# Optimization experiments

Hardware: AMD Instinct MI355X
Metric: run time of the kernel (lower is better)

Reference implementation:

```python
import jax, jax.numpy as jnp
import numpy as np

N_NODES = 81920
N_EDGES = 1310720
NODES_PER_GRAPH = 320
N_GRAPHS = N_NODES // NODES_PER_GRAPH  # 256
IN_DIM = 64
HID = 64
OUT = 64


def setup_inputs() -> dict:
    key = jax.random.key(0)
    ks = jax.random.split(key, 16)
    x = jax.random.normal(ks[0], (N_NODES, IN_DIM), dtype=jnp.float32)
    edge_index = jax.random.randint(ks[1], (2, N_EDGES), 0, N_NODES, dtype=jnp.int32)
    # sorted graph-membership vector: 256 graphs of 320 nodes each
    batch = (jnp.arange(N_NODES, dtype=jnp.int32) // NODES_PER_GRAPH)
    std = 1.0  # module re-inits nn.Linear weights with N(0, 1)
    dims = [(IN_DIM, HID), (HID, HID), (HID, OUT)]
    params = {}
    for i, (di, do) in enumerate(dims):
        params[f"Wl{i}"] = std * jax.random.normal(ks[2 + 3 * i], (di, do), dtype=jnp.float32)
        params[f"bl{i}"] = jnp.zeros((do,), dtype=jnp.float32)
        params[f"Wr{i}"] = std * jax.random.normal(ks[3 + 3 * i], (di, do), dtype=jnp.float32)
    return dict(x=x, edge_index=edge_index, batch=batch, **params)


def _sage_conv(x, src, dst, Wl, bl, Wr):
    # PyG SAGEConv (aggr='mean', root_weight=True):
    #   out = lin_l(mean_{j in N(i)} x_j) + lin_r(x_i)
    msg = x[src]                                              # [E, d] gather
    agg = jax.ops.segment_sum(msg, dst, num_segments=N_NODES)  # [N, d] scatter-add
    cnt = jax.ops.segment_sum(jnp.ones((src.shape[0],), x.dtype), dst,
                              num_segments=N_NODES)
    agg = agg / jnp.maximum(cnt, 1.0)[:, None]                # mean aggregation
    return agg @ Wl + bl + x @ Wr


def reference(x, edge_index, batch, Wl0, bl0, Wr0, Wl1, bl1, Wr1, Wl2, bl2, Wr2):
    src, dst = edge_index[0], edge_index[1]
    layers = [(Wl0, bl0, Wr0), (Wl1, bl1, Wr1), (Wl2, bl2, Wr2)]
    h = x
    for i, (Wl, bl, Wr) in enumerate(layers):
        h = _sage_conv(h, src, dst, Wl, bl, Wr)
        if i < len(layers) - 1:
            h = jax.nn.relu(h)
            # F.dropout is identity in eval mode (training=False)
    # unbatch + take node 0 of every graph: first index where batch == g
    first_idx = jnp.searchsorted(batch, jnp.arange(N_GRAPHS, dtype=batch.dtype))
    return h[first_idx]  # [N_GRAPHS, OUT]
```

## Files before the change

### kernel.cpp

```cpp
#include <hip/hip_runtime.h>

#define N_NODES 81920
#define N_EDGES 1310720
#define NG 256
#define D 64
#define TM 64
#define SA 65
#define SB 33
#define NB 320
#define NBLK 1280
#define BMW 2560
#define HCHUNK 4096
#define EPT 16
#define CAP0 1280
#define CAP1 256
#define CAP2 64

typedef __attribute__((ext_vector_type(2))) short sbf2;

__device__ __forceinline__ bool tb(const unsigned* bm, int i) {
    return (bm[i >> 5] >> (i & 31)) & 1u;
}
__device__ __forceinline__ unsigned bf16rne(float f) {
    unsigned u = __float_as_uint(f);
    return (u + 0x7fffu + ((u >> 16) & 1u)) >> 16;
}


__global__ __launch_bounds__(256) void init_ws(float4* __restrict__ aggb4,
                                               unsigned* __restrict__ bms,
                                               int* __restrict__ indeg,
                                               int* __restrict__ n01,
                                               int* __restrict__ cur0,
                                               int* __restrict__ cur1,
                                               int* __restrict__ cur2) {
    int t = blockIdx.x * 256 + threadIdx.x;
    float4 z = make_float4(0.f, 0.f, 0.f, 0.f);
    aggb4[t] = z;
    aggb4[t + NBLK * 256] = z;
    if (t < 3 * BMW) bms[t] = 0u;
    if (t < N_NODES) indeg[t] = 0;
    if (t < 2) n01[t] = 0;
    if (t < NBLK) {
        cur0[t] = t * CAP0;
        cur1[t] = t * CAP1;
        cur2[t] = t * CAP2;
    }
}


__global__ void ff_mark(const int* __restrict__ batch, int* __restrict__ fidx,
                        unsigned* __restrict__ bm2, unsigned* __restrict__ bm1,
                        float* __restrict__ aggf) {
    int i = blockIdx.x * 256 + threadIdx.x;
    int b = batch[i];
    if (i == 0 || batch[i - 1] != b) {
        fidx[b] = i;
        unsigned bit = 1u << (i & 31);
        atomicOr(&bm2[i >> 5], bit);
        atomicOr(&bm1[i >> 5], bit);
        float4* r = (float4*)&aggf[i * D];
        #pragma unroll
        for (int j = 0; j < 16; ++j) r[j] = make_float4(0.f, 0.f, 0.f, 0.f);
    }
}

__global__ void mark_srcs_bm(const int* __restrict__ src, const int* __restrict__ dst,
                             const unsigned* __restrict__ bmD, unsigned* __restrict__ bmS,
                             const unsigned* __restrict__ orsrc) {
    if (orsrc && blockIdx.x == 0) {
        for (int w = threadIdx.x; w < BMW; w += 256)
            if (orsrc[w]) atomicOr(&bmS[w], orsrc[w]);
    }
    int e = blockIdx.x * 256 + threadIdx.x;
    if (e < N_EDGES && tb(bmD, dst[e])) {
        int s = src[e];
        atomicOr(&bmS[s >> 5], 1u << (s & 31));
    }
}


__global__ __launch_bounds__(256) void build(const int* __restrict__ src,
                                             const int* __restrict__ dst,
                                             const unsigned* __restrict__ bm0,
                                             const unsigned* __restrict__ bm1,
                                             const unsigned* __restrict__ bm2,
                                             int* __restrict__ cur0,
                                             int* __restrict__ cur1,
                                             int* __restrict__ cur2,
                                             int* __restrict__ esp0,
                                             int* __restrict__ esp1,
                                             int* __restrict__ esp2,
                                             int* __restrict__ indeg,
                                             int* __restrict__ list1,
                                             int* __restrict__ n1) {
    __shared__ int h0[NBLK];
    __shared__ int b0[NBLK];
    const int tid = threadIdx.x;
    const int e0  = blockIdx.x * HCHUNK;

    for (int i = tid; i < NBLK; i += 256) h0[i] = 0;

    {
        int i = blockIdx.x * 256 + tid;
        int lane = tid & 63;
        bool p1 = tb(bm1, i);
        unsigned long long b1 = __ballot(p1);
        int lt = __popcll(b1 & ((1ull << lane) - 1));
        int base = 0;
        if (lane == 0 && b1) base = atomicAdd(n1, __popcll(b1));
        base = __shfl(base, 0);
        if (p1) list1[base + lt] = i;
    }
    __syncthreads();

    int pk_r[EPT];
    int sb_r[EPT];
    int rk_r[EPT];

    #pragma unroll
    for (int j = 0; j < EPT; ++j) {
        int e = e0 + j * 256 + tid;
        int d = dst[e];
        sb_r[j] = -1;
        if (tb(bm0, d)) {
            int s  = src[e];
            int sb = s >> 6;
            int pk = (d << 6) | (s & 63);
            pk_r[j] = pk;
            sb_r[j] = sb;
            rk_r[j] = atomicAdd(&h0[sb], 1);
            atomicAdd(&indeg[d], 1);
            if (tb(bm1, d)) {
                int p1 = atomicAdd(&cur1[sb], 1);
                if (p1 < sb * CAP1 + CAP1) esp1[p1] = pk;
                if (tb(bm2, d)) {
                    int p2 = atomicAdd(&cur2[sb], 1);
                    if (p2 < sb * CAP2 + CAP2) esp2[p2] = pk;
                }
            }
        }
    }
    __syncthreads();

    for (int i = tid; i < NBLK; i += 256) {
        int c = h0[i];
        b0[i] = c ? atomicAdd(&cur0[i], c) : 0;
    }
    __syncthreads();

    #pragma unroll
    for (int j = 0; j < EPT; ++j) {
        int sb = sb_r[j];
        if (sb >= 0) {
            int pos = b0[sb] + rk_r[j];
            if (pos < sb * CAP0 + CAP0) esp0[pos] = pk_r[j];
        }
    }
}


__global__ __launch_bounds__(256, 8) void sage_push_bf(
    const float* __restrict__ hin, const int* __restrict__ cur,
    const int* __restrict__ esp, unsigned* __restrict__ aggb, int cap)
{
    __shared__ unsigned Rs[TM * SB];

    const int tid  = threadIdx.x;
    const int base = blockIdx.x * TM;
    const int lane = tid & 63;
    const int w    = tid >> 6;
    const int l5   = lane & 31;
    const int hi   = lane >> 5;

    const int e0 = blockIdx.x * cap;
    const int e1 = min(cur[blockIdx.x], e0 + cap);
    if (e0 == e1) return;

    for (int idx = tid; idx < TM * 32; idx += 256) {
        int m = idx >> 5, k = idx & 31;
        float2 v = *(const float2*)&hin[((base + m) << 6) + (k << 1)];
        Rs[m * SB + k] = bf16rne(v.x) | (bf16rne(v.y) << 16);
    }
    __syncthreads();

    const int chunk = ((e1 - e0) + 3) >> 2;
    int e = e0 + w * chunk;
    const int ee = min(e + chunk, e1);

    for (; e + 64 <= ee; e += 64) {
        int pv = esp[e + lane];
        #pragma unroll
        for (int u = 0; u < 32; ++u) {
            int p = __shfl(pv, (u << 1) + hi);
            unsigned v = Rs[(p & 63) * SB + l5];
            __builtin_amdgcn_global_atomic_fadd_v2bf16(
                (sbf2*)&aggb[((p >> 6) << 5) + l5], *(sbf2*)&v);
        }
    }
    for (; e < ee; ++e) {
        int p = esp[e];
        if (!hi) {
            unsigned v = Rs[(p & 63) * SB + l5];
            __builtin_amdgcn_global_atomic_fadd_v2bf16(
                (sbf2*)&aggb[((p >> 6) << 5) + l5], *(sbf2*)&v);
        }
    }
}


__global__ __launch_bounds__(256, 8) void sage_push_f32(
    const float* __restrict__ hin, const int* __restrict__ cur,
    const int* __restrict__ esp, float* __restrict__ agg, int cap)
{
    __shared__ float Rs[TM * SA];

    const int tid  = threadIdx.x;
    const int base = blockIdx.x * TM;
    const int lane = tid & 63;
    const int w    = tid >> 6;

    const int e0 = blockIdx.x * cap;
    const int e1 = min(cur[blockIdx.x], e0 + cap);
    if (e0 == e1) return;

    for (int idx = tid; idx < TM * D; idx += 256) {
        int m = idx >> 6, k = idx & 63;
        Rs[m * SA + k] = hin[(base << 6) + idx];
    }
    __syncthreads();

    const int chunk = ((e1 - e0) + 3) >> 2;
    int e = e0 + w * chunk;
    const int ee = min(e + chunk, e1);

    for (; e < ee; ++e) {
        int p = esp[e];
        atomicAdd(&agg[(p & 0x7fffffc0) + lane], Rs[(p & 63) * SA + lane]);
    }
}


__global__ __launch_bounds__(256, 4) void sage_finish_dense(
    const float* __restrict__ hin, unsigned* __restrict__ aggb,
    const int* __restrict__ indeg, float* __restrict__ hout,
    const float* __restrict__ Wl, const float* __restrict__ bl,
    const float* __restrict__ Wr)
{
    __shared__ float As[TM * SA];
    __shared__ float Xs[TM * SA];
    __shared__ float invs[TM];

    const int tid  = threadIdx.x;
    const int base = blockIdx.x * TM;

    if (tid < TM) invs[tid] = 1.0f / (float)max(indeg[base + tid], 1);
    for (int idx = tid; idx < TM * 32; idx += 256) {
        int m = idx >> 5, k2 = idx & 31;
        unsigned v = aggb[(base << 5) + idx];
        As[m * SA + (k2 << 1)]     = __uint_as_float(v << 16);
        As[m * SA + (k2 << 1) + 1] = __uint_as_float(v & 0xffff0000u);
        aggb[(base << 5) + idx] = 0u;
    }
    for (int idx = tid; idx < TM * D; idx += 256) {
        int m = idx >> 6, k = idx & 63;
        Xs[m * SA + k] = hin[(base << 6) + idx];
    }
    __syncthreads();
    for (int idx = tid; idx < TM * D; idx += 256) {
        int m = idx >> 6, k = idx & 63;
        As[m * SA + k] *= invs[m];
    }
    __syncthreads();

    const int j0 = (tid & 15) << 2;
    const int m0 = (tid >> 4) << 2;
    float o[4][4];
    float4 b4 = *(const float4*)&bl[j0];
    #pragma unroll
    for (int mi = 0; mi < 4; ++mi) {
        o[mi][0] = b4.x; o[mi][1] = b4.y; o[mi][2] = b4.z; o[mi][3] = b4.w;
    }
    #pragma unroll 8
    for (int k = 0; k < D; ++k) {
        float4 wl = *(const float4*)&Wl[(k << 6) + j0];
        float4 wr = *(const float4*)&Wr[(k << 6) + j0];
        #pragma unroll
        for (int mi = 0; mi < 4; ++mi) {
            float a = As[(m0 + mi) * SA + k];
            float x = Xs[(m0 + mi) * SA + k];
            o[mi][0] += a * wl.x + x * wr.x;
            o[mi][1] += a * wl.y + x * wr.y;
            o[mi][2] += a * wl.z + x * wr.z;
            o[mi][3] += a * wl.w + x * wr.w;
        }
    }
    #pragma unroll
    for (int mi = 0; mi < 4; ++mi) {
        float4 r = make_float4(fmaxf(o[mi][0], 0.f), fmaxf(o[mi][1], 0.f),
                               fmaxf(o[mi][2], 0.f), fmaxf(o[mi][3], 0.f));
        *(float4*)&hout[(base + m0 + mi) * D + j0] = r;
    }
}


__global__ __launch_bounds__(256, 4) void sage_finish_sel(
    const float* __restrict__ hin, unsigned* __restrict__ aggb,
    const int* __restrict__ indeg, const int* __restrict__ list,
    const int* __restrict__ pcount, float* __restrict__ hout,
    const float* __restrict__ Wl, const float* __restrict__ bl,
    const float* __restrict__ Wr)
{
    __shared__ float As[TM * SA];
    __shared__ float Xs[TM * SA];
    __shared__ float invs[TM];
    __shared__ int   nid[TM];

    const int cntv = *pcount;
    const int base = blockIdx.x * TM;
    if (base >= cntv) return;

    const int tid = threadIdx.x;
    if (tid < TM) {
        int n = (base + tid < cntv) ? list[base + tid] : -1;
        nid[tid]  = n;
        invs[tid] = (n >= 0) ? 1.0f / (float)max(indeg[n], 1) : 0.f;
    }
    __syncthreads();
    for (int idx = tid; idx < TM * 32; idx += 256) {
        int m = idx >> 5, k2 = idx & 31;
        int n = nid[m];
        if (n >= 0) {
            unsigned v = aggb[(n << 5) + k2];
            As[m * SA + (k2 << 1)]     = __uint_as_float(v << 16) * invs[m];
            As[m * SA + (k2 << 1) + 1] = __uint_as_float(v & 0xffff0000u) * invs[m];
        } else {
            As[m * SA + (k2 << 1)]     = 0.f;
            As[m * SA + (k2 << 1) + 1] = 0.f;
        }
    }
    for (int idx = tid; idx < TM * D; idx += 256) {
        int m = idx >> 6, k = idx & 63;
        int n = nid[m];
        Xs[m * SA + k] = (n >= 0) ? hin[n * D + k] : 0.f;
    }
    __syncthreads();

    const int j0 = (tid & 15) << 2;
    const int m0 = (tid >> 4) << 2;
    float o[4][4];
    float4 b4 = *(const float4*)&bl[j0];
    #pragma unroll
    for (int mi = 0; mi < 4; ++mi) {
        o[mi][0] = b4.x; o[mi][1] = b4.y; o[mi][2] = b4.z; o[mi][3] = b4.w;
    }
    #pragma unroll 8
    for (int k = 0; k < D; ++k) {
        float4 wl = *(const float4*)&Wl[(k << 6) + j0];
        float4 wr = *(const float4*)&Wr[(k << 6) + j0];
        #pragma unroll
        for (int mi = 0; mi < 4; ++mi) {
            float a = As[(m0 + mi) * SA + k];
            float x = Xs[(m0 + mi) * SA + k];
            o[mi][0] += a * wl.x + x * wr.x;
            o[mi][1] += a * wl.y + x * wr.y;
            o[mi][2] += a * wl.z + x * wr.z;
            o[mi][3] += a * wl.w + x * wr.w;
        }
    }
    #pragma unroll
    for (int mi = 0; mi < 4; ++mi) {
        int n = nid[m0 + mi];
        if (n >= 0) {
            float4 r = make_float4(fmaxf(o[mi][0], 0.f), fmaxf(o[mi][1], 0.f),
                                   fmaxf(o[mi][2], 0.f), fmaxf(o[mi][3], 0.f));
            *(float4*)&hout[n * D + j0] = r;
        }
    }
}


__global__ __launch_bounds__(256, 3) void final_gemm_sel(
    const float* __restrict__ hin, const float* __restrict__ agg,
    const int* __restrict__ indeg, const int* __restrict__ fidx,
    const float* __restrict__ Wl, const float* __restrict__ bl,
    const float* __restrict__ Wr, float* __restrict__ out)
{
    __shared__ float As[TM * SA];
    __shared__ float Xs[TM * SA];
    __shared__ int   nid[TM];
    __shared__ float invs[TM];

    const int tid  = threadIdx.x;
    const int base = blockIdx.x * TM;

    if (tid < TM) {
        int n = fidx[base + tid];
        nid[tid]  = n;
        invs[tid] = 1.0f / (float)max(indeg[n], 1);
    }
    __syncthreads();
    for (int idx = tid; idx < TM * D; idx += 256) {
        int m = idx >> 6, k = idx & 63;
        int n = nid[m];
        As[m * SA + k] = agg[n * D + k] * invs[m];
        Xs[m * SA + k] = hin[n * D + k];
    }
    __syncthreads();

    const int j0 = (tid & 15) << 2;
    const int m0 = (tid >> 4) << 2;
    float o[4][4];
    float4 b4 = *(const float4*)&bl[j0];
    #pragma unroll
    for (int mi = 0; mi < 4; ++mi) {
        o[mi][0] = b4.x; o[mi][1] = b4.y; o[mi][2] = b4.z; o[mi][3] = b4.w;
    }
    #pragma unroll 8
    for (int k = 0; k < D; ++k) {
        float4 wl = *(const float4*)&Wl[(k << 6) + j0];
        float4 wr = *(const float4*)&Wr[(k << 6) + j0];
        #pragma unroll
        for (int mi = 0; mi < 4; ++mi) {
            float a = As[(m0 + mi) * SA + k];
            float x = Xs[(m0 + mi) * SA + k];
            o[mi][0] += a * wl.x + x * wr.x;
            o[mi][1] += a * wl.y + x * wr.y;
            o[mi][2] += a * wl.z + x * wr.z;
            o[mi][3] += a * wl.w + x * wr.w;
        }
    }
    #pragma unroll
    for (int mi = 0; mi < 4; ++mi) {
        float4 r = make_float4(o[mi][0], o[mi][1], o[mi][2], o[mi][3]);
        *(float4*)&out[(base + m0 + mi) * D + j0] = r;
    }
}


extern "C" void kernel_launch(void* const* d_in, const int* in_sizes, int n_in,
                              void* d_out, int out_size, void* d_ws, size_t ws_size,
                              hipStream_t stream)
{
    const float* x     = (const float*)d_in[0];
    const int*   ei    = (const int*)d_in[1];
    const int*   batch = (const int*)d_in[2];
    const float* Wl0 = (const float*)d_in[3];
    const float* bl0 = (const float*)d_in[4];
    const float* Wr0 = (const float*)d_in[5];
    const float* Wl1 = (const float*)d_in[6];
    const float* bl1 = (const float*)d_in[7];
    const float* Wr1 = (const float*)d_in[8];
    const float* Wl2 = (const float*)d_in[9];
    const float* bl2 = (const float*)d_in[10];
    const float* Wr2 = (const float*)d_in[11];
    float* out = (float*)d_out;

    const int* src = ei;
    const int* dst = ei + N_EDGES;

    char* ws = (char*)d_ws;
    size_t off = 0;
    auto alloc = [&](size_t bytes) -> void* {
        void* p = ws + off;
        off = (off + bytes + 255) & ~(size_t)255;
        return p;
    };
    int*      cur0  = (int*)alloc(NBLK * sizeof(int));
    int*      cur1  = (int*)alloc(NBLK * sizeof(int));
    int*      cur2  = (int*)alloc(NBLK * sizeof(int));
    int*      fidx  = (int*)alloc(NG * sizeof(int));
    int*      list1 = (int*)alloc(N_NODES * sizeof(int));
    int*      esp0  = (int*)alloc((size_t)NBLK * CAP0 * sizeof(int));
    int*      esp1  = (int*)alloc((size_t)NBLK * CAP1 * sizeof(int));
    int*      esp2  = (int*)alloc((size_t)NBLK * CAP2 * sizeof(int));
    unsigned* aggb  = (unsigned*)alloc((size_t)N_NODES * 32 * sizeof(unsigned));
    float*    aggf  = (float*)alloc((size_t)N_NODES * D * sizeof(float));
    float*    h1    = (float*)alloc((size_t)N_NODES * D * sizeof(float));
    float*    h2    = (float*)alloc((size_t)N_NODES * D * sizeof(float));
    unsigned* bms   = (unsigned*)alloc((size_t)3 * BMW * sizeof(unsigned));
    int*      indeg = (int*)alloc(N_NODES * sizeof(int));
    int*      n01   = (int*)alloc(64 * sizeof(int));
    unsigned* bm0 = bms;
    unsigned* bm1 = bms + BMW;
    unsigned* bm2 = bms + 2 * BMW;
    int* n1 = n01 + 1;
    (void)ws_size; (void)in_sizes; (void)n_in; (void)out_size;

    const int EB = (N_EDGES + 255) / 256;

    init_ws<<<NBLK, 256, 0, stream>>>((float4*)aggb, bms, indeg, n01, cur0, cur1, cur2);
    ff_mark<<<NB, 256, 0, stream>>>(batch, fidx, bm2, bm1, aggf);
    mark_srcs_bm<<<EB, 256, 0, stream>>>(src, dst, bm2, bm1, (const unsigned*)nullptr);
    mark_srcs_bm<<<EB, 256, 0, stream>>>(src, dst, bm1, bm0, bm1);
    build<<<NB, 256, 0, stream>>>(src, dst, bm0, bm1, bm2, cur0, cur1, cur2,
                                  esp0, esp1, esp2, indeg, list1, n1);

    sage_push_bf     <<<NBLK, 256, 0, stream>>>(x, cur0, esp0, aggb, CAP0);
    sage_finish_dense<<<NBLK, 256, 0, stream>>>(x, aggb, indeg, h1, Wl0, bl0, Wr0);
    sage_push_bf     <<<NBLK, 256, 0, stream>>>(h1, cur1, esp1, aggb, CAP1);
    sage_finish_sel  <<<NBLK, 256, 0, stream>>>(h1, aggb, indeg, list1, n1,
                                                h2, Wl1, bl1, Wr1);
    sage_push_f32    <<<NBLK, 256, 0, stream>>>(h2, cur2, esp2, aggf, CAP2);
    final_gemm_sel   <<<NG / TM, 256, 0, stream>>>(h2, aggf, indeg, fidx, Wl2, bl2, Wr2, out);
}
```

Before: 404.5 us.

## Bucket layer-0 edges by destination and fuse pull aggregation with dense GEMM

Layer-0 edges are now bucketed by destination block instead of source block. A new pull kernel gathers source rows from global memory, accumulates them into shared memory with LDS float atomics, counts in-degree locally, and runs the dense linear transform in the same kernel. This removes the global bf16 atomics, the aggb zero/readback pass, the separate finish kernel and the global indeg atomics in build. In exchange it adds uncoalesced per-edge global gathers of x rows and contention on LDS atomics. Layer-0 accumulation is now in fp32 instead of bf16.

```diff
diff --git a/kernel.cpp b/kernel.cpp
--- a/kernel.cpp
+++ b/kernel.cpp
@@ -91,7 +91,6 @@
                                              int* __restrict__ esp0,
                                              int* __restrict__ esp1,
                                              int* __restrict__ esp2,
-                                             int* __restrict__ indeg,
                                              int* __restrict__ list1,
                                              int* __restrict__ n1) {
     __shared__ int h0[NBLK];
@@ -115,23 +114,23 @@
     __syncthreads();
 
     int pk_r[EPT];
-    int sb_r[EPT];
+    int db_r[EPT];
     int rk_r[EPT];
 
     #pragma unroll
     for (int j = 0; j < EPT; ++j) {
         int e = e0 + j * 256 + tid;
         int d = dst[e];
-        sb_r[j] = -1;
+        db_r[j] = -1;
         if (tb(bm0, d)) {
             int s  = src[e];
-            int sb = s >> 6;
-            int pk = (d << 6) | (s & 63);
-            pk_r[j] = pk;
-            sb_r[j] = sb;
-            rk_r[j] = atomicAdd(&h0[sb], 1);
-            atomicAdd(&indeg[d], 1);
+            int db = d >> 6;
+            pk_r[j] = (s << 6) | (d & 63);
+            db_r[j] = db;
+            rk_r[j] = atomicAdd(&h0[db], 1);
             if (tb(bm1, d)) {
+                int sb = s >> 6;
+                int pk = (d << 6) | (s & 63);
                 int p1 = atomicAdd(&cur1[sb], 1);
                 if (p1 < sb * CAP1 + CAP1) esp1[p1] = pk;
                 if (tb(bm2, d)) {
@@ -151,120 +150,72 @@
 
     #pragma unroll
     for (int j = 0; j < EPT; ++j) {
-        int sb = sb_r[j];
-        if (sb >= 0) {
-            int pos = b0[sb] + rk_r[j];
-            if (pos < sb * CAP0 + CAP0) esp0[pos] = pk_r[j];
-        }
-    }
-}
-
-
-__global__ __launch_bounds__(256, 8) void sage_push_bf(
-    const float* __restrict__ hin, const int* __restrict__ cur,
-    const int* __restrict__ esp, unsigned* __restrict__ aggb, int cap)
-{
-    __shared__ unsigned Rs[TM * SB];
-
-    const int tid  = threadIdx.x;
-    const int base = blockIdx.x * TM;
-    const int lane = tid & 63;
-    const int w    = tid >> 6;
-    const int l5   = lane & 31;
-    const int hi   = lane >> 5;
-
-    const int e0 = blockIdx.x * cap;
-    const int e1 = min(cur[blockIdx.x], e0 + cap);
-    if (e0 == e1) return;
-
-    for (int idx = tid; idx < TM * 32; idx += 256) {
-        int m = idx >> 5, k = idx & 31;
-        float2 v = *(const float2*)&hin[((base + m) << 6) + (k << 1)];
-        Rs[m * SB + k] = bf16rne(v.x) | (bf16rne(v.y) << 16);
-    }
-    __syncthreads();
-
-    const int chunk = ((e1 - e0) + 3) >> 2;
-    int e = e0 + w * chunk;
-    const int ee = min(e + chunk, e1);
-
-    for (; e + 64 <= ee; e += 64) {
-        int pv = esp[e + lane];
-        #pragma unroll
-        for (int u = 0; u < 32; ++u) {
-            int p = __shfl(pv, (u << 1) + hi);
-            unsigned v = Rs[(p & 63) * SB + l5];
-            __builtin_amdgcn_global_atomic_fadd_v2bf16(
-                (sbf2*)&aggb[((p >> 6) << 5) + l5], *(sbf2*)&v);
-        }
-    }
-    for (; e < ee; ++e) {
-        int p = esp[e];
-        if (!hi) {
-            unsigned v = Rs[(p & 63) * SB + l5];
-            __builtin_amdgcn_global_atomic_fadd_v2bf16(
-                (sbf2*)&aggb[((p >> 6) << 5) + l5], *(sbf2*)&v);
-        }
-    }
-}
-
-
-__global__ __launch_bounds__(256, 8) void sage_push_f32(
-    const float* __restrict__ hin, const int* __restrict__ cur,
-    const int* __restrict__ esp, float* __restrict__ agg, int cap)
-{
-    __shared__ float Rs[TM * SA];
-
-    const int tid  = threadIdx.x;
-    const int base = blockIdx.x * TM;
-    const int lane = tid & 63;
-    const int w    = tid >> 6;
-
-    const int e0 = blockIdx.x * cap;
-    const int e1 = min(cur[blockIdx.x], e0 + cap);
-    if (e0 == e1) return;
-
-    for (int idx = tid; idx < TM * D; idx += 256) {
-        int m = idx >> 6, k = idx & 63;
-        Rs[m * SA + k] = hin[(base << 6) + idx];
-    }
-    __syncthreads();
-
-    const int chunk = ((e1 - e0) + 3) >> 2;
-    int e = e0 + w * chunk;
-    const int ee = min(e + chunk, e1);
-
-    for (; e < ee; ++e) {
-        int p = esp[e];
-        atomicAdd(&agg[(p & 0x7fffffc0) + lane], Rs[(p & 63) * SA + lane]);
-    }
-}
-
-
-__global__ __launch_bounds__(256, 4) void sage_finish_dense(
-    const float* __restrict__ hin, unsigned* __restrict__ aggb,
-    const int* __restrict__ indeg, float* __restrict__ hout,
+        int db = db_r[j];
+        if (db >= 0) {
+            int pos = b0[db] + rk_r[j];
+            if (pos < db * CAP0 + CAP0) esp0[pos] = pk_r[j];
+        }
+    }
+}
+
+
+__global__ __launch_bounds__(256, 4) void sage_pull_l0(
+    const float* __restrict__ xin, const int* __restrict__ cur,
+    const int* __restrict__ esp, int* __restrict__ indeg,
+    float* __restrict__ hout,
     const float* __restrict__ Wl, const float* __restrict__ bl,
     const float* __restrict__ Wr)
 {
     __shared__ float As[TM * SA];
     __shared__ float Xs[TM * SA];
+    __shared__ int   cw[4 * TM];
     __shared__ float invs[TM];
 
     const int tid  = threadIdx.x;
     const int base = blockIdx.x * TM;
-
-    if (tid < TM) invs[tid] = 1.0f / (float)max(indeg[base + tid], 1);
-    for (int idx = tid; idx < TM * 32; idx += 256) {
-        int m = idx >> 5, k2 = idx & 31;
-        unsigned v = aggb[(base << 5) + idx];
-        As[m * SA + (k2 << 1)]     = __uint_as_float(v << 16);
-        As[m * SA + (k2 << 1) + 1] = __uint_as_float(v & 0xffff0000u);
-        aggb[(base << 5) + idx] = 0u;
-    }
+    const int lane = tid & 63;
+    const int w    = tid >> 6;
+
     for (int idx = tid; idx < TM * D; idx += 256) {
         int m = idx >> 6, k = idx & 63;
-        Xs[m * SA + k] = hin[(base << 6) + idx];
+        Xs[m * SA + k] = xin[(base << 6) + idx];
+        As[m * SA + k] = 0.f;
+    }
+    __syncthreads();
+
+    const int e0 = blockIdx.x * CAP0;
+    const int e1 = min(cur[blockIdx.x], e0 + CAP0);
+
+    const int chunk = ((e1 - e0) + 3) >> 2;
+    int e = e0 + w * chunk;
+    const int ee = min(e + chunk, e1);
+
+    int cnt = 0;
+    for (; e + 64 <= ee; e += 64) {
+        int pv = esp[e + lane];
+        #pragma unroll
+        for (int u = 0; u < 64; ++u) {
+            int p  = __builtin_amdgcn_readlane(pv, u);
+            int dl = p & 63;
+            float v = xin[((p >> 6) << 6) + lane];
+            atomicAdd(&As[dl * SA + lane], v);
+            cnt += (lane == dl) ? 1 : 0;
+        }
+    }
+    for (; e < ee; ++e) {
+        int p  = esp[e];
+        int dl = p & 63;
+        float v = xin[((p >> 6) << 6) + lane];
+        atomicAdd(&As[dl * SA + lane], v);
+        cnt += (lane == dl) ? 1 : 0;
+    }
+    cw[w * TM + lane] = cnt;
+    __syncthreads();
+
+    if (tid < TM) {
+        int c = cw[tid] + cw[TM + tid] + cw[2 * TM + tid] + cw[3 * TM + tid];
+        indeg[base + tid] = c;
+        invs[tid] = 1.0f / (float)max(c, 1);
     }
     __syncthreads();
     for (int idx = tid; idx < TM * D; idx += 256) {
@@ -300,6 +251,87 @@
         float4 r = make_float4(fmaxf(o[mi][0], 0.f), fmaxf(o[mi][1], 0.f),
                                fmaxf(o[mi][2], 0.f), fmaxf(o[mi][3], 0.f));
         *(float4*)&hout[(base + m0 + mi) * D + j0] = r;
+    }
+}
+
+
+__global__ __launch_bounds__(256, 8) void sage_push_bf(
+    const float* __restrict__ hin, const int* __restrict__ cur,
+    const int* __restrict__ esp, unsigned* __restrict__ aggb, int cap)
+{
+    __shared__ unsigned Rs[TM * SB];
+
+    const int tid  = threadIdx.x;
+    const int base = blockIdx.x * TM;
+    const int lane = tid & 63;
+    const int w    = tid >> 6;
+    const int l5   = lane & 31;
+    const int hi   = lane >> 5;
+
+    const int e0 = blockIdx.x * cap;
+    const int e1 = min(cur[blockIdx.x], e0 + cap);
+    if (e0 == e1) return;
+
+    for (int idx = tid; idx < TM * 32; idx += 256) {
+        int m = idx >> 5, k = idx & 31;
+        float2 v = *(const float2*)&hin[((base + m) << 6) + (k << 1)];
+        Rs[m * SB + k] = bf16rne(v.x) | (bf16rne(v.y) << 16);
+    }
+    __syncthreads();
+
+    const int chunk = ((e1 - e0) + 3) >> 2;
+    int e = e0 + w * chunk;
+    const int ee = min(e + chunk, e1);
+
+    for (; e + 64 <= ee; e += 64) {
+        int pv = esp[e + lane];
+        #pragma unroll
+        for (int u = 0; u < 32; ++u) {
+            int p = __shfl(pv, (u << 1) + hi);
+            unsigned v = Rs[(p & 63) * SB + l5];
+            __builtin_amdgcn_global_atomic_fadd_v2bf16(
+                (sbf2*)&aggb[((p >> 6) << 5) + l5], *(sbf2*)&v);
+        }
+    }
+    for (; e < ee; ++e) {
+        int p = esp[e];
+        if (!hi) {
+            unsigned v = Rs[(p & 63) * SB + l5];
+            __builtin_amdgcn_global_atomic_fadd_v2bf16(
+                (sbf2*)&aggb[((p >> 6) << 5) + l5], *(sbf2*)&v);
+        }
+    }
+}
+
+
+__global__ __launch_bounds__(256, 8) void sage_push_f32(
+    const float* __restrict__ hin, const int* __restrict__ cur,
+    const int* __restrict__ esp, float* __restrict__ agg, int cap)
+{
+    __shared__ float Rs[TM * SA];
+
+    const int tid  = threadIdx.x;
+    const int base = blockIdx.x * TM;
+    const int lane = tid & 63;
+    const int w    = tid >> 6;
+
+    const int e0 = blockIdx.x * cap;
+    const int e1 = min(cur[blockIdx.x], e0 + cap);
+    if (e0 == e1) return;
+
+    for (int idx = tid; idx < TM * D; idx += 256) {
+        int m = idx >> 6, k = idx & 63;
+        Rs[m * SA + k] = hin[(base << 6) + idx];
+    }
+    __syncthreads();
+
+    const int chunk = ((e1 - e0) + 3) >> 2;
+    int e = e0 + w * chunk;
+    const int ee = min(e + chunk, e1);
+
+    for (; e < ee; ++e) {
+        int p = esp[e];
+        atomicAdd(&agg[(p & 0x7fffffc0) + lane], Rs[(p & 63) * SA + lane]);
     }
 }
 
@@ -494,10 +526,9 @@
     mark_srcs_bm<<<EB, 256, 0, stream>>>(src, dst, bm2, bm1, (const unsigned*)nullptr);
     mark_srcs_bm<<<EB, 256, 0, stream>>>(src, dst, bm1, bm0, bm1);
     build<<<NB, 256, 0, stream>>>(src, dst, bm0, bm1, bm2, cur0, cur1, cur2,
-                                  esp0, esp1, esp2, indeg, list1, n1);
-
-    sage_push_bf     <<<NBLK, 256, 0, stream>>>(x, cur0, esp0, aggb, CAP0);
-    sage_finish_dense<<<NBLK, 256, 0, stream>>>(x, aggb, indeg, h1, Wl0, bl0, Wr0);
+                                  esp0, esp1, esp2, list1, n1);
+
+    sage_pull_l0<<<NBLK, 256, 0, stream>>>(x, cur0, esp0, indeg, h1, Wl0, bl0, Wr0);
     sage_push_bf     <<<NBLK, 256, 0, stream>>>(h1, cur1, esp1, aggb, CAP1);
     sage_finish_sel  <<<NBLK, 256, 0, stream>>>(h1, aggb, indeg, list1, n1,
                                                 h2, Wl1, bl1, Wr1);
```

Measured after the change: 533.0 us. 1.32x slower.
